# Optimization experiments

Hardware: AMD Instinct MI355X
Metric: run time of the kernel (lower is better)

## Reference

```python
import jax, jax.numpy as jnp
import numpy as np

H, KVH, DH = 16, 4, 64
DIM = 1024
SCALE_BASE = 4096  # context_len
EPS = 1e-6


def rmsnorm(x, g):
    return x * jax.lax.rsqrt(jnp.mean(x * x, axis=-1, keepdims=True) + EPS) * g


def rope_tables(n, dh, dtype):
    inv_freq = 1.0 / (10000.0 ** (jnp.arange(0, dh, 2, dtype=jnp.float32) / dh))
    t = jnp.arange(n, dtype=jnp.float32) * (SCALE_BASE / n)
    freqs = t[:, None] * inv_freq[None, :]          # [n, dh/2]
    emb = jnp.concatenate([freqs, freqs], axis=-1)  # [n, dh]
    return jnp.cos(emb).astype(dtype), jnp.sin(emb).astype(dtype)


def apply_rope(x, cos, sin):
    # x: [b, h, n, dh]; cos/sin: [n, dh]
    x1, x2 = jnp.split(x, 2, axis=-1)
    rot = jnp.concatenate([-x2, x1], axis=-1)
    return x * cos + rot * sin


def setup_inputs() -> dict:
    key = jax.random.key(0)
    ks = jax.random.split(key, 12)
    B, N = 1, 2048
    std = 0.02
    inp = {
        "x": jax.random.normal(ks[0], (B, N, DIM), jnp.float32),
        "a": jax.random.normal(ks[1], (B, N, DIM), jnp.float32),
        "g_x": jnp.ones((DIM,), jnp.float32),
        "g_a": jnp.ones((DIM,), jnp.float32),
        "Wq_x": jax.random.normal(ks[2], (DIM, H * DH), jnp.float32) * std,
        "Wkv_x": jax.random.normal(ks[3], (DIM, 2 * KVH * DH), jnp.float32) * std,
        "Wq_a": jax.random.normal(ks[4], (DIM, H * DH), jnp.float32) * std,
        "Wkv_a": jax.random.normal(ks[5], (DIM, 2 * KVH * DH), jnp.float32) * std,
        "Wout_x": jax.random.normal(ks[6], (H * DH, DIM), jnp.float32) * std,
        "bout_x": jnp.zeros((DIM,), jnp.float32),
        "Wout_a": jax.random.normal(ks[7], (H * DH, DIM), jnp.float32) * std,
        "bout_a": jnp.zeros((DIM,), jnp.float32),
    }
    return inp


def _split_heads(t, h):
    b, n, hd = t.shape
    return t.reshape(b, n, h, hd // h).transpose(0, 2, 1, 3)  # b h n d


def _stream_qkv(s, g, Wq, Wkv):
    s = rmsnorm(s, g)
    q = _split_heads(s @ Wq, H)                 # [b, H, n, DH]
    kv = s @ Wkv
    k, v = jnp.split(kv, 2, axis=-1)
    k = _split_heads(k, KVH)                    # [b, KVH, n, DH]
    v = _split_heads(v, KVH)
    return q, k, v


def reference(x, a, g_x, g_a, Wq_x, Wkv_x, Wq_a, Wkv_a, Wout_x, bout_x, Wout_a, bout_a):
    B, Nx, _ = x.shape
    Na = a.shape[1]
    scale = DH ** -0.5
    r = H // KVH

    q_x, k_x, v_x = _stream_qkv(x, g_x, Wq_x, Wkv_x)
    q_a, k_a, v_a = _stream_qkv(a, g_a, Wq_a, Wkv_a)

    cos_x, sin_x = rope_tables(Nx, DH, x.dtype)
    cos_a, sin_a = rope_tables(Na, DH, a.dtype)
    q_x, k_x = apply_rope(q_x, cos_x, sin_x), apply_rope(k_x, cos_x, sin_x)
    q_a, k_a = apply_rope(q_a, cos_a, sin_a), apply_rope(k_a, cos_a, sin_a)

    # NOTE: original scales q by dim_head**-0.5 AND sdpa scales again -> 1/DH total
    q_x = q_x * scale
    q_a = q_a * scale

    # GQA expansion: einops 'b h n d -> b (r h) n d' == tile heads
    tile = lambda t: jnp.tile(t, (1, r, 1, 1))
    k_x, v_x, k_a, v_a = tile(k_x), tile(v_x), tile(k_a), tile(v_a)

    # pack [a, x] along seq
    q = jnp.concatenate([q_a, q_x], axis=2)
    k = jnp.concatenate([k_a, k_x], axis=2)
    v = jnp.concatenate([v_a, v_x], axis=2)

    scores = jnp.einsum('bhqd,bhkd->bhqk', q, k) * scale  # sdpa's own scale
    attn = jax.nn.softmax(scores, axis=-1)
    out = jnp.einsum('bhqk,bhkd->bhqd', attn, v)          # [b, H, Na+Nx, DH]

    out_a, out_x = out[:, :, :Na], out[:, :, Na:]
    merge = lambda t: t.transpose(0, 2, 1, 3).reshape(B, -1, H * DH)
    out_x = merge(out_x) @ Wout_x + bout_x
    out_a = merge(out_a) @ Wout_a + bout_a
    return out_x, out_a
```

## Files before the change

### kernel.cpp

```cpp
#include <hip/hip_runtime.h>
#include <hip/hip_bf16.h>
#include <stdint.h>
#include <math.h>


#define NSEQ 2048
#define NJ   4096
#define DIMM 1024

typedef __attribute__((ext_vector_type(4))) float f32x4;
typedef __attribute__((ext_vector_type(8))) short bf16x8;
typedef __attribute__((ext_vector_type(4))) short bf16x4;

__device__ __forceinline__ unsigned short f2bf(float f) {
  union { float f; uint32_t u; } v; v.f = f;
  return (unsigned short)((v.u + 0x7FFFu + ((v.u >> 16) & 1u)) >> 16);
}

__device__ __forceinline__ uint32_t pack2bf(float a, float b) {
  __hip_bfloat162 h = __float22bfloat162_rn(float2{a, b});
  union { __hip_bfloat162 h; uint32_t u; } c; c.h = h;
  return c.u;
}

#if defined(__has_builtin)
#if __has_builtin(__builtin_amdgcn_exp2f)
#define FAST_EXP2(x) __builtin_amdgcn_exp2f(x)
#endif
#endif
#ifndef FAST_EXP2
#define FAST_EXP2(x) exp2f(x)
#endif

__device__ __forceinline__ void glds16(const void* g, void* l) {
  __builtin_amdgcn_global_load_lds(
      (const __attribute__((address_space(1))) unsigned int*)g,
      (__attribute__((address_space(3))) unsigned int*)l, 16, 0, 0);
}

__global__ __launch_bounds__(256) void prep_kernel(
    const float* __restrict__ xa, const float* __restrict__ xx,
    const float* __restrict__ ga, const float* __restrict__ gx,
    const float* __restrict__ wqa, const float* __restrict__ wqx,
    const float* __restrict__ wkva, const float* __restrict__ wkvx,
    const float* __restrict__ woa, const float* __restrict__ wox,
    unsigned short* __restrict__ XN, unsigned short* __restrict__ WQT,
    unsigned short* __restrict__ WKVT, unsigned short* __restrict__ WOT,
    float* __restrict__ cosT, float* __restrict__ sinT) {
  __shared__ float tile[32][33];
  __shared__ float red[4];
  int bid = blockIdx.x, t = threadIdx.x;
  if (bid < 256) {
    int idx = bid * 256 + t;
    int pos = idx >> 5, i = idx & 31;
    double inv = pow(10000.0, -(double)i / 32.0);
    double ang = (double)(2 * pos) * inv;
    cosT[idx] = (float)cos(ang);
    sinT[idx] = (float)sin(ang);
  } else if (bid < 6400) {
    int b = bid - 256;
    int z = b >> 10, yx = b & 1023;
    int n0 = (yx >> 5) * 32, k0 = (yx & 31) * 32;
    int s = z & 1, ty = z >> 1;
    int N = (ty == 1) ? 512 : 1024;
    if (n0 >= N) return;
    const float* src = (z == 0) ? wqa : (z == 1) ? wqx : (z == 2) ? wkva
                     : (z == 3) ? wkvx : (z == 4) ? woa : wox;
    unsigned short* dst = (ty == 0) ? WQT + (size_t)s * 1024 * 1024
                        : (ty == 1) ? WKVT + (size_t)s * 512 * 1024
                                    : WOT + (size_t)s * 1024 * 1024;
    int r = t >> 3, c4 = (t & 7) * 4;
    f32x4 v = *(const f32x4*)(src + (size_t)(k0 + r) * N + n0 + c4);
    tile[r][c4 + 0] = v.x; tile[r][c4 + 1] = v.y;
    tile[r][c4 + 2] = v.z; tile[r][c4 + 3] = v.w;
    __syncthreads();
    int nn = t >> 3, kk = (t & 7) * 4;
    bf16x4 o;
    o.x = (short)f2bf(tile[kk + 0][nn]);
    o.y = (short)f2bf(tile[kk + 1][nn]);
    o.z = (short)f2bf(tile[kk + 2][nn]);
    o.w = (short)f2bf(tile[kk + 3][nn]);
    *(bf16x4*)(dst + (size_t)(n0 + nn) * 1024 + k0 + kk) = o;
  } else {
    int b = bid - 6400;
    int s = b >> 11, row = b & 2047;
    const float* src = (s == 0 ? xa : xx) + (size_t)row * DIMM;
    const float* g = (s == 0 ? ga : gx);
    f32x4 v = *(const f32x4*)(src + t * 4);
    float ss = v.x * v.x + v.y * v.y + v.z * v.z + v.w * v.w;
#pragma unroll
    for (int o = 32; o > 0; o >>= 1) ss += __shfl_xor(ss, o, 64);
    if ((t & 63) == 0) red[t >> 6] = ss;
    __syncthreads();
    float tot = red[0] + red[1] + red[2] + red[3];
    float rs = rsqrtf(tot * (1.0f / DIMM) + 1e-6f);
    f32x4 gv = *(const f32x4*)(g + t * 4);
    bf16x4 o;
    o.x = (short)f2bf(v.x * rs * gv.x);
    o.y = (short)f2bf(v.y * rs * gv.y);
    o.z = (short)f2bf(v.z * rs * gv.z);
    o.w = (short)f2bf(v.w * rs * gv.w);
    *(bf16x4*)(XN + ((size_t)s * NSEQ + row) * DIMM + t * 4) = o;
  }
}

__device__ __forceinline__ void gemm64_mainloop(
    const unsigned short* __restrict__ Ag, const unsigned short* __restrict__ Bg,
    unsigned short* As, unsigned short* Bs, f32x4 acc[2][4]) {
  int t = threadIdx.x;
  int lane = t & 63, wid = t >> 6;
  int wm = (wid >> 1) * 32, wn = (wid & 1) * 64;
  int l15 = lane & 15, quad = lane >> 4;
  int srow = t >> 2, sko = (t & 3) * 8;
  const unsigned short* ga = Ag + (size_t)srow * 1024 + sko;
  const unsigned short* gb = Bg + (size_t)srow * 1024 + sko;
  unsigned short* la = As + t * 8;
  unsigned short* lb = Bs + t * 8;
#pragma unroll
  for (int mi = 0; mi < 2; ++mi)
#pragma unroll
    for (int j = 0; j < 4; ++j) acc[mi][j] = (f32x4){0.f, 0.f, 0.f, 0.f};

#define GQ_STAGE(S, KT) do {                                               \
    int k0_ = (KT) * 32;                                                   \
    glds16(ga + k0_, la + (S) * 2048);                                     \
    glds16(gb + k0_, lb + (S) * 4096);                                     \
    glds16(gb + 64 * 1024 + k0_, lb + (S) * 4096 + 2048);                  \
  } while (0)

#define GQ_COMP(S) do {                                                    \
    bf16x8 af[2], bfr[4];                                                  \
    _Pragma("unroll")                                                      \
    for (int mi = 0; mi < 2; ++mi)                                         \
      af[mi] = *(const bf16x8*)(As + (S) * 2048 + (wm + mi * 16 + l15) * 32 + quad * 8); \
    _Pragma("unroll")                                                      \
    for (int j = 0; j < 4; ++j)                                            \
      bfr[j] = *(const bf16x8*)(Bs + (S) * 4096 + (wn + j * 16 + l15) * 32 + quad * 8); \
    _Pragma("unroll")                                                      \
    for (int mi = 0; mi < 2; ++mi)                                         \
      _Pragma("unroll")                                                    \
      for (int j = 0; j < 4; ++j)                                          \
        acc[mi][j] = __builtin_amdgcn_mfma_f32_16x16x32_bf16(af[mi], bfr[j], acc[mi][j], 0, 0, 0); \
  } while (0)

  GQ_STAGE(0, 0);
  GQ_STAGE(1, 1);
  __syncthreads();
  for (int kq = 0; kq < 32; kq += 4) {
    GQ_STAGE(2, (kq + 2) & 31);
    GQ_STAGE(3, (kq + 3) & 31);
    GQ_COMP(0);
    GQ_COMP(1);
    __syncthreads();
    GQ_STAGE(0, (kq + 4) & 31);
    GQ_STAGE(1, (kq + 5) & 31);
    GQ_COMP(2);
    GQ_COMP(3);
    __syncthreads();
  }
#undef GQ_STAGE
#undef GQ_COMP
}

__global__ __launch_bounds__(256) void gemm_qkv_kernel(
    const unsigned short* __restrict__ XN, const unsigned short* __restrict__ WQT,
    const unsigned short* __restrict__ WKVT, const float* __restrict__ cosT,
    const float* __restrict__ sinT, unsigned short* __restrict__ QB,
    unsigned short* __restrict__ KB, unsigned short* __restrict__ VT) {
  __shared__ unsigned short As[4 * 2048], Bs[4 * 4096];
  int n0 = blockIdx.x * 128, m0 = blockIdx.y * 64;
  int s = (m0 >= 2048) ? 1 : 0;
  const unsigned short* Ag = XN + (size_t)m0 * 1024;
  const unsigned short* Bg = (n0 < 1024)
      ? WQT + (size_t)s * 1024 * 1024 + (size_t)n0 * 1024
      : WKVT + (size_t)s * 512 * 1024 + (size_t)(n0 - 1024) * 1024;
  f32x4 acc[2][4];
  gemm64_mainloop(Ag, Bg, As, Bs, acc);
  int t = threadIdx.x, lane = t & 63, wid = t >> 6;
  int wm = (wid >> 1) * 32, wn = (wid & 1) * 64;
  int l15 = lane & 15, quad = lane >> 4;
  int coln = n0 + wn;
  if (coln < 1280) {
    bool isq = coln < 1024;
    float sc = isq ? (1.4426950408889634f / 64.0f) : 1.0f;
    unsigned short* dstBase;
    if (isq) dstBase = QB + (size_t)(coln >> 6) * NJ * 64;
    else     dstBase = KB + (size_t)((coln - 1024) >> 6) * NJ * 64;
#pragma unroll
    for (int mi = 0; mi < 2; ++mi)
#pragma unroll
      for (int r = 0; r < 4; ++r) {
        int jr = m0 + wm + mi * 16 + quad * 4 + r;
        int pos = jr & 2047;
#pragma unroll
        for (int jp = 0; jp < 2; ++jp) {
          int i = jp * 16 + l15;
          float c = cosT[pos * 32 + i], sn = sinT[pos * 32 + i];
          float x1 = acc[mi][jp][r], x2 = acc[mi][jp + 2][r];
          dstBase[(size_t)jr * 64 + jp * 16 + l15]      = f2bf((x1 * c - x2 * sn) * sc);
          dstBase[(size_t)jr * 64 + 32 + jp * 16 + l15] = f2bf((x2 * c + x1 * sn) * sc);
        }
      }
  } else {
    int cvb = coln - 1280;
#pragma unroll
    for (int mi = 0; mi < 2; ++mi)
#pragma unroll
      for (int j = 0; j < 4; ++j) {
        int d = cvb + j * 16 + l15;
        int jr0 = m0 + wm + mi * 16 + quad * 4;
        union { bf16x4 v; uint32_t u[2]; } pv;
        pv.u[0] = pack2bf(acc[mi][j][0], acc[mi][j][1]);
        pv.u[1] = pack2bf(acc[mi][j][2], acc[mi][j][3]);
        *(bf16x4*)(VT + (size_t)d * NJ + jr0) = pv.v;
      }
  }
}

__global__ __launch_bounds__(256, 2) void attn_kernel(
    const unsigned short* __restrict__ QB, const unsigned short* __restrict__ KB,
    const unsigned short* __restrict__ VT, unsigned short* __restrict__ AT) {
  __shared__ __align__(16) unsigned short Ks[4][4096];
  __shared__ __align__(16) unsigned short Vs[4][4096];
  int h = blockIdx.y, qt = blockIdx.x;
  int hk = h & 3;
  int t = threadIdx.x, lane = t & 63, w = t >> 6;
  int l15 = lane & 15, quad = lane >> 4;
  int qsel = w >> 1, ksel = w & 1;
  int q0 = qt * 128 + qsel * 64;
  bf16x8 qf[4][2];
#pragma unroll
  for (int mi = 0; mi < 4; ++mi) {
    const unsigned short* qp = QB + ((size_t)h * NJ + q0 + mi * 16 + l15) * 64;
    qf[mi][0] = *(const bf16x8*)(qp + quad * 8);
    qf[mi][1] = *(const bf16x8*)(qp + 32 + quad * 8);
  }
  f32x4 oT[4][4];
  f32x4 oL[4];
#pragma unroll
  for (int mi = 0; mi < 4; ++mi) {
    oL[mi] = (f32x4){0.f, 0.f, 0.f, 0.f};
#pragma unroll
    for (int db = 0; db < 4; ++db) oT[mi][db] = (f32x4){0.f, 0.f, 0.f, 0.f};
  }
  bf16x8 vone;
  {
    short one = (l15 == 0) ? (short)0x3F80 : (short)0;
    vone = (bf16x8){one, one, one, one, one, one, one, one};
  }
  const unsigned short* Kg = KB + (size_t)hk * NJ * 64;
  const unsigned short* Vg = VT + (size_t)hk * 64 * NJ;
  int r1 = t >> 3, cx = t & 7;
  int e1 = r1 & 7;
  int c1 = cx ^ e1;
  int gk1 = 32 * (r1 >> 5) + 8 * ((r1 >> 2) & 3) + 4 * ((r1 >> 4) & 1) + (r1 & 3);
  int r2 = r1 + 32;
  int gk2 = 32 * (r2 >> 5) + 8 * ((r2 >> 2) & 3) + 4 * ((r2 >> 4) & 1) + (r2 & 3);
  const unsigned short* sK1 = Kg + (size_t)gk1 * 64 + c1 * 8;
  const unsigned short* sK2 = Kg + (size_t)gk2 * 64 + c1 * 8;
  const unsigned short* sV1 = Vg + (size_t)r1 * NJ + c1 * 8;
  const unsigned short* sV2 = Vg + (size_t)r2 * NJ + c1 * 8;
  int e = l15 & 7;
  int co0 = (quad ^ e) * 8;
  int co1 = ((4 + quad) ^ e) * 8;
  int cov = (((ksel << 2) | quad) ^ e) * 8;
  const unsigned short* kf0p = &Ks[0][(2 * ksel * 16 + l15) * 64] + co0;
  const unsigned short* kf0q = &Ks[0][(2 * ksel * 16 + l15) * 64] + co1;
  const unsigned short* kf1p = kf0p + 16 * 64;
  const unsigned short* kf1q = kf0q + 16 * 64;
  const unsigned short* vap0 = &Vs[0][(0 * 16 + l15) * 64] + cov;
  const unsigned short* vap1 = &Vs[0][(1 * 16 + l15) * 64] + cov;
  const unsigned short* vap2 = &Vs[0][(2 * 16 + l15) * 64] + cov;
  const unsigned short* vap3 = &Vs[0][(3 * 16 + l15) * 64] + cov;

  f32x4 sxA[4][2], sxB[4][2];
  bf16x8 pbA[4], pbB[4];

#define STAGE(S, T) do {                                                   \
    size_t ko_ = (size_t)(T) * 4096;                                       \
    int vo_ = (T) * 64;                                                    \
    glds16(sK1 + ko_, &Ks[S][0] + t * 8);                                  \
    glds16(sK2 + ko_, &Ks[S][2048] + t * 8);                               \
    glds16(sV1 + vo_, &Vs[S][0] + t * 8);                                  \
    glds16(sV2 + vo_, &Vs[S][2048] + t * 8);                               \
  } while (0)

#define QK4(S, SX) do {                                                    \
    bf16x8 k00 = *(const bf16x8*)(kf0p + (S) * 4096);                      \
    bf16x8 k01 = *(const bf16x8*)(kf0q + (S) * 4096);                      \
    bf16x8 k10 = *(const bf16x8*)(kf1p + (S) * 4096);                      \
    bf16x8 k11 = *(const bf16x8*)(kf1q + (S) * 4096);                      \
    _Pragma("unroll")                                                      \
    for (int mi = 0; mi < 4; ++mi) {                                       \
      f32x4 z0 = (f32x4){0.f, 0.f, 0.f, 0.f};                              \
      z0 = __builtin_amdgcn_mfma_f32_16x16x32_bf16(k00, qf[mi][0], z0, 0, 0, 0); \
      z0 = __builtin_amdgcn_mfma_f32_16x16x32_bf16(k01, qf[mi][1], z0, 0, 0, 0); \
      (SX)[mi][0] = z0;                                                    \
      f32x4 z1 = (f32x4){0.f, 0.f, 0.f, 0.f};                              \
      z1 = __builtin_amdgcn_mfma_f32_16x16x32_bf16(k10, qf[mi][0], z1, 0, 0, 0); \
      z1 = __builtin_amdgcn_mfma_f32_16x16x32_bf16(k11, qf[mi][1], z1, 0, 0, 0); \
      (SX)[mi][1] = z1;                                                    \
    }                                                                      \
  } while (0)

#define PHASE_A(SQ, SXN, SXP, PB) do {                                     \
    bf16x8 k00 = *(const bf16x8*)(kf0p + (SQ) * 4096);                     \
    bf16x8 k01 = *(const bf16x8*)(kf0q + (SQ) * 4096);                     \
    bf16x8 k10 = *(const bf16x8*)(kf1p + (SQ) * 4096);                     \
    bf16x8 k11 = *(const bf16x8*)(kf1q + (SQ) * 4096);                     \
    _Pragma("unroll")                                                      \
    for (int mi = 0; mi < 4; ++mi) {                                       \
      f32x4 z0 = (f32x4){0.f, 0.f, 0.f, 0.f};                              \
      z0 = __builtin_amdgcn_mfma_f32_16x16x32_bf16(k00, qf[mi][0], z0, 0, 0, 0); \
      z0 = __builtin_amdgcn_mfma_f32_16x16x32_bf16(k01, qf[mi][1], z0, 0, 0, 0); \
      (SXN)[mi][0] = z0;                                                   \
      f32x4 z1 = (f32x4){0.f, 0.f, 0.f, 0.f};                              \
      z1 = __builtin_amdgcn_mfma_f32_16x16x32_bf16(k10, qf[mi][0], z1, 0, 0, 0); \
      z1 = __builtin_amdgcn_mfma_f32_16x16x32_bf16(k11, qf[mi][1], z1, 0, 0, 0); \
      (SXN)[mi][1] = z1;                                                   \
      union { bf16x8 v; uint32_t u[4]; } pk_;                              \
      pk_.u[0] = pack2bf(FAST_EXP2((SXP)[mi][0][0]), FAST_EXP2((SXP)[mi][0][1])); \
      pk_.u[1] = pack2bf(FAST_EXP2((SXP)[mi][0][2]), FAST_EXP2((SXP)[mi][0][3])); \
      pk_.u[2] = pack2bf(FAST_EXP2((SXP)[mi][1][0]), FAST_EXP2((SXP)[mi][1][1])); \
      pk_.u[3] = pack2bf(FAST_EXP2((SXP)[mi][1][2]), FAST_EXP2((SXP)[mi][1][3])); \
      (PB)[mi] = pk_.v;                                                    \
    }                                                                      \
  } while (0)

#define PHASE_C(SP, PB, SX, PBN) do {                                      \
    bf16x8 va0 = *(const bf16x8*)(vap0 + (SP) * 4096);                     \
    bf16x8 va1 = *(const bf16x8*)(vap1 + (SP) * 4096);                     \
    bf16x8 va2 = *(const bf16x8*)(vap2 + (SP) * 4096);                     \
    bf16x8 va3 = *(const bf16x8*)(vap3 + (SP) * 4096);                     \
    _Pragma("unroll")                                                      \
    for (int mi = 0; mi < 4; ++mi) {                                       \
      oT[mi][0] = __builtin_amdgcn_mfma_f32_16x16x32_bf16(va0, (PB)[mi], oT[mi][0], 0, 0, 0); \
      oT[mi][1] = __builtin_amdgcn_mfma_f32_16x16x32_bf16(va1, (PB)[mi], oT[mi][1], 0, 0, 0); \
      oT[mi][2] = __builtin_amdgcn_mfma_f32_16x16x32_bf16(va2, (PB)[mi], oT[mi][2], 0, 0, 0); \
      oT[mi][3] = __builtin_amdgcn_mfma_f32_16x16x32_bf16(va3, (PB)[mi], oT[mi][3], 0, 0, 0); \
      oL[mi]    = __builtin_amdgcn_mfma_f32_16x16x32_bf16(vone, (PB)[mi], oL[mi], 0, 0, 0); \
      union { bf16x8 v; uint32_t u[4]; } pk_;                              \
      pk_.u[0] = pack2bf(FAST_EXP2((SX)[mi][0][0]), FAST_EXP2((SX)[mi][0][1])); \
      pk_.u[1] = pack2bf(FAST_EXP2((SX)[mi][0][2]), FAST_EXP2((SX)[mi][0][3])); \
      pk_.u[2] = pack2bf(FAST_EXP2((SX)[mi][1][0]), FAST_EXP2((SX)[mi][1][1])); \
      pk_.u[3] = pack2bf(FAST_EXP2((SX)[mi][1][2]), FAST_EXP2((SX)[mi][1][3])); \
      (PBN)[mi] = pk_.v;                                                   \
    }                                                                      \
  } while (0)

#define PHASE_B(SP, PB) do {                                               \
    __builtin_amdgcn_s_setprio(1);                                         \
    {                                                                      \
      bf16x8 va0 = *(const bf16x8*)(vap0 + (SP) * 4096);                   \
      bf16x8 va1 = *(const bf16x8*)(vap1 + (SP) * 4096);                   \
      bf16x8 va2 = *(const bf16x8*)(vap2 + (SP) * 4096);                   \
      bf16x8 va3 = *(const bf16x8*)(vap3 + (SP) * 4096);                   \
      _Pragma("unroll")                                                    \
      for (int mi = 0; mi < 4; ++mi) {                                     \
        oT[mi][0] = __builtin_amdgcn_mfma_f32_16x16x32_bf16(va0, (PB)[mi], oT[mi][0], 0, 0, 0); \
        oT[mi][1] = __builtin_amdgcn_mfma_f32_16x16x32_bf16(va1, (PB)[mi], oT[mi][1], 0, 0, 0); \
        oT[mi][2] = __builtin_amdgcn_mfma_f32_16x16x32_bf16(va2, (PB)[mi], oT[mi][2], 0, 0, 0); \
        oT[mi][3] = __builtin_amdgcn_mfma_f32_16x16x32_bf16(va3, (PB)[mi], oT[mi][3], 0, 0, 0); \
        oL[mi]    = __builtin_amdgcn_mfma_f32_16x16x32_bf16(vone, (PB)[mi], oL[mi], 0, 0, 0); \
      }                                                                    \
    }                                                                      \
    __builtin_amdgcn_s_setprio(0);                                         \
  } while (0)

  STAGE(0, 0);
  STAGE(1, 1);
  __syncthreads();
  for (int P = 0; P < 16; ++P) {
    int tb = 4 * P;
    STAGE(2, (tb + 2) & 63);
    STAGE(3, (tb + 3) & 63);
    QK4(0, sxA);
    PHASE_A(1, sxB, sxA, pbA);
    PHASE_C(0, pbA, sxB, pbB);
    PHASE_B(1, pbB);
    __syncthreads();
    STAGE(0, (tb + 4) & 63);
    STAGE(1, (tb + 5) & 63);
    QK4(2, sxA);
    PHASE_A(3, sxB, sxA, pbA);
    PHASE_C(2, pbA, sxB, pbB);
    PHASE_B(3, pbB);
    __syncthreads();
  }
#undef STAGE
#undef QK4
#undef PHASE_A
#undef PHASE_C
#undef PHASE_B

  float ls[4];
#pragma unroll
  for (int mi = 0; mi < 4; ++mi) {
    float s = oL[mi][0];
    s += __shfl_xor(s, 16, 64);
    s += __shfl_xor(s, 32, 64);
    ls[mi] = s;
  }
  float* xb = (qsel == 0) ? (float*)&Ks[0][0] : (float*)&Vs[0][0];
  float* xl = xb + 64 * 68;
  if (ksel == 1) {
    f32x4* dst = (f32x4*)xb + (size_t)lane * 17;
#pragma unroll
    for (int mi = 0; mi < 4; ++mi)
#pragma unroll
      for (int db = 0; db < 4; ++db) dst[mi * 4 + db] = oT[mi][db];
    float* dl = xl + lane * 4;
#pragma unroll
    for (int mi = 0; mi < 4; ++mi) dl[mi] = ls[mi];
  }
  __syncthreads();
  if (ksel == 0) {
    const f32x4* src = (const f32x4*)xb + (size_t)lane * 17;
    const float* sl = xl + lane * 4;
#pragma unroll
    for (int mi = 0; mi < 4; ++mi) {
      float inv = 1.0f / (ls[mi] + sl[mi]);
      int qrow = q0 + mi * 16 + l15;
#pragma unroll
      for (int db = 0; db < 4; ++db) {
        f32x4 o = oT[mi][db] + src[mi * 4 + db];
        union { bf16x4 v; uint32_t u[2]; } ov;
        ov.u[0] = pack2bf(o[0] * inv, o[1] * inv);
        ov.u[1] = pack2bf(o[2] * inv, o[3] * inv);
        *(bf16x4*)(AT + (size_t)qrow * DIMM + h * 64 + db * 16 + quad * 4) = ov.v;
      }
    }
  }
}

__global__ __launch_bounds__(256) void gemm_out_kernel(
    const unsigned short* __restrict__ AT, const unsigned short* __restrict__ WOT,
    const float* __restrict__ ba, const float* __restrict__ bx,
    float* __restrict__ out) {
  __shared__ unsigned short As[4 * 2048], Bs[4 * 4096];
  int n0 = blockIdx.x * 128, m0 = blockIdx.y * 64;
  int s = (m0 >= 2048) ? 1 : 0;
  const unsigned short* Ag = AT + (size_t)m0 * 1024;
  const unsigned short* Bg = WOT + (size_t)s * 1024 * 1024 + (size_t)n0 * 1024;
  f32x4 acc[2][4];
  gemm64_mainloop(Ag, Bg, As, Bs, acc);
  int t = threadIdx.x, lane = t & 63, wid = t >> 6;
  int wm = (wid >> 1) * 32, wn = (wid & 1) * 64;
  int l15 = lane & 15, quad = lane >> 4;
  const float* bias = s ? bx : ba;
  float* obase = s ? (out + (size_t)(m0 - 2048) * 1024)
                   : (out + (size_t)2048 * 1024 + (size_t)m0 * 1024);
#pragma unroll
  for (int mi = 0; mi < 2; ++mi)
#pragma unroll
    for (int r = 0; r < 4; ++r) {
      int row = wm + mi * 16 + quad * 4 + r;
#pragma unroll
      for (int j = 0; j < 4; ++j) {
        int col = n0 + wn + j * 16 + l15;
        obase[(size_t)row * 1024 + col] = acc[mi][j][r] + bias[col];
      }
    }
}

extern "C" void kernel_launch(void* const* d_in, const int* in_sizes, int n_in,
                              void* d_out, int out_size, void* d_ws, size_t ws_size,
                              hipStream_t stream) {
  const float* x      = (const float*)d_in[0];
  const float* a      = (const float*)d_in[1];
  const float* g_x    = (const float*)d_in[2];
  const float* g_a    = (const float*)d_in[3];
  const float* Wq_x   = (const float*)d_in[4];
  const float* Wkv_x  = (const float*)d_in[5];
  const float* Wq_a   = (const float*)d_in[6];
  const float* Wkv_a  = (const float*)d_in[7];
  const float* Wout_x = (const float*)d_in[8];
  const float* bout_x = (const float*)d_in[9];
  const float* Wout_a = (const float*)d_in[10];
  const float* bout_a = (const float*)d_in[11];
  float* out = (float*)d_out;

  char* ws = (char*)d_ws;
  const size_t MB = 1024 * 1024;
  unsigned short* XN   = (unsigned short*)(ws);
  unsigned short* WQT  = (unsigned short*)(ws + 8 * MB);
  unsigned short* WKVT = (unsigned short*)(ws + 12 * MB);
  unsigned short* WOT  = (unsigned short*)(ws + 14 * MB);
  unsigned short* QB   = (unsigned short*)(ws + 18 * MB);
  unsigned short* KB   = (unsigned short*)(ws + 26 * MB);
  unsigned short* VT   = (unsigned short*)(ws + 28 * MB);
  float* cosT          = (float*)(ws + 30 * MB);
  float* sinT          = (float*)(ws + 30 * MB + 262144);
  unsigned short* AT   = XN;

  prep_kernel<<<dim3(10496), dim3(256), 0, stream>>>(
      a, x, g_a, g_x, Wq_a, Wq_x, Wkv_a, Wkv_x, Wout_a, Wout_x,
      XN, WQT, WKVT, WOT, cosT, sinT);
  gemm_qkv_kernel<<<dim3(12, 64), dim3(256), 0, stream>>>(
      XN, WQT, WKVT, cosT, sinT, QB, KB, VT);
  attn_kernel<<<dim3(32, 16), dim3(256), 0, stream>>>(QB, KB, VT, AT);
  gemm_out_kernel<<<dim3(8, 64), dim3(256), 0, stream>>>(
      AT, WOT, bout_a, bout_x, out);
}
```

Baseline: 218.3 us.

## Restructure attention loop into continuous software pipeline and use hardware sin/cos for RoPE

The attention main loop is rebuilt as a steady-state software pipeline. QK for the next tile is computed alongside the exp and PV of the previous tile, with one barrier per tile instead of a burst of two stages per barrier, and a single P buffer replaces the two. This aims to overlap MFMA work with the softmax exponentials and spread LDS staging more evenly, but doubles the number of barriers. Separately, the RoPE table prep swaps double-precision pow/sin/cos for a bitwise product of constants and the hardware v_sin/v_cos instructions, cutting prep cost at some loss of precision.

```diff
diff --git a/kernel.cpp b/kernel.cpp
--- a/kernel.cpp
+++ b/kernel.cpp
@@ -53,10 +53,21 @@
   if (bid < 256) {
     int idx = bid * 256 + t;
     int pos = idx >> 5, i = idx & 31;
-    double inv = pow(10000.0, -(double)i / 32.0);
+    double inv = 1.0;
+    if (i & 1)  inv *= 0.74989420933245582;
+    if (i & 2)  inv *= 0.56234132519034908;
+    if (i & 4)  inv *= 0.31622776601683794;
+    if (i & 8)  inv *= 0.1;
+    if (i & 16) inv *= 0.01;
     double ang = (double)(2 * pos) * inv;
-    cosT[idx] = (float)cos(ang);
-    sinT[idx] = (float)sin(ang);
+    double rev = ang * 0.15915494309189535;
+    rev -= floor(rev);
+    float rf = (float)rev;
+    float c, s;
+    asm("v_cos_f32 %0, %1" : "=v"(c) : "v"(rf));
+    asm("v_sin_f32 %0, %1" : "=v"(s) : "v"(rf));
+    cosT[idx] = c;
+    sinT[idx] = s;
   } else if (bid < 6400) {
     int b = bid - 256;
     int z = b >> 10, yx = b & 1023;
@@ -274,7 +285,7 @@
   const unsigned short* vap3 = &Vs[0][(3 * 16 + l15) * 64] + cov;
 
   f32x4 sxA[4][2], sxB[4][2];
-  bf16x8 pbA[4], pbB[4];
+  bf16x8 pb[4];
 
 #define STAGE(S, T) do {                                                   \
     size_t ko_ = (size_t)(T) * 4096;                                       \
@@ -303,7 +314,7 @@
     }                                                                      \
   } while (0)
 
-#define PHASE_A(SQ, SXN, SXP, PB) do {                                     \
+#define PHASE_A(SQ, SXN, SXP) do {                                         \
     bf16x8 k00 = *(const bf16x8*)(kf0p + (SQ) * 4096);                     \
     bf16x8 k01 = *(const bf16x8*)(kf0q + (SQ) * 4096);                     \
     bf16x8 k10 = *(const bf16x8*)(kf1p + (SQ) * 4096);                     \
@@ -323,32 +334,11 @@
       pk_.u[1] = pack2bf(FAST_EXP2((SXP)[mi][0][2]), FAST_EXP2((SXP)[mi][0][3])); \
       pk_.u[2] = pack2bf(FAST_EXP2((SXP)[mi][1][0]), FAST_EXP2((SXP)[mi][1][1])); \
       pk_.u[3] = pack2bf(FAST_EXP2((SXP)[mi][1][2]), FAST_EXP2((SXP)[mi][1][3])); \
-      (PB)[mi] = pk_.v;                                                    \
+      pb[mi] = pk_.v;                                                      \
     }                                                                      \
   } while (0)
 
-#define PHASE_C(SP, PB, SX, PBN) do {                                      \
-    bf16x8 va0 = *(const bf16x8*)(vap0 + (SP) * 4096);                     \
-    bf16x8 va1 = *(const bf16x8*)(vap1 + (SP) * 4096);                     \
-    bf16x8 va2 = *(const bf16x8*)(vap2 + (SP) * 4096);                     \
-    bf16x8 va3 = *(const bf16x8*)(vap3 + (SP) * 4096);                     \
-    _Pragma("unroll")                                                      \
-    for (int mi = 0; mi < 4; ++mi) {                                       \
-      oT[mi][0] = __builtin_amdgcn_mfma_f32_16x16x32_bf16(va0, (PB)[mi], oT[mi][0], 0, 0, 0); \
-      oT[mi][1] = __builtin_amdgcn_mfma_f32_16x16x32_bf16(va1, (PB)[mi], oT[mi][1], 0, 0, 0); \
-      oT[mi][2] = __builtin_amdgcn_mfma_f32_16x16x32_bf16(va2, (PB)[mi], oT[mi][2], 0, 0, 0); \
-      oT[mi][3] = __builtin_amdgcn_mfma_f32_16x16x32_bf16(va3, (PB)[mi], oT[mi][3], 0, 0, 0); \
-      oL[mi]    = __builtin_amdgcn_mfma_f32_16x16x32_bf16(vone, (PB)[mi], oL[mi], 0, 0, 0); \
-      union { bf16x8 v; uint32_t u[4]; } pk_;                              \
-      pk_.u[0] = pack2bf(FAST_EXP2((SX)[mi][0][0]), FAST_EXP2((SX)[mi][0][1])); \
-      pk_.u[1] = pack2bf(FAST_EXP2((SX)[mi][0][2]), FAST_EXP2((SX)[mi][0][3])); \
-      pk_.u[2] = pack2bf(FAST_EXP2((SX)[mi][1][0]), FAST_EXP2((SX)[mi][1][1])); \
-      pk_.u[3] = pack2bf(FAST_EXP2((SX)[mi][1][2]), FAST_EXP2((SX)[mi][1][3])); \
-      (PBN)[mi] = pk_.v;                                                   \
-    }                                                                      \
-  } while (0)
-
-#define PHASE_B(SP, PB) do {                                               \
+#define PHASE_B(SP) do {                                                   \
     __builtin_amdgcn_s_setprio(1);                                         \
     {                                                                      \
       bf16x8 va0 = *(const bf16x8*)(vap0 + (SP) * 4096);                   \
@@ -357,11 +347,11 @@
       bf16x8 va3 = *(const bf16x8*)(vap3 + (SP) * 4096);                   \
       _Pragma("unroll")                                                    \
       for (int mi = 0; mi < 4; ++mi) {                                     \
-        oT[mi][0] = __builtin_amdgcn_mfma_f32_16x16x32_bf16(va0, (PB)[mi], oT[mi][0], 0, 0, 0); \
-        oT[mi][1] = __builtin_amdgcn_mfma_f32_16x16x32_bf16(va1, (PB)[mi], oT[mi][1], 0, 0, 0); \
-        oT[mi][2] = __builtin_amdgcn_mfma_f32_16x16x32_bf16(va2, (PB)[mi], oT[mi][2], 0, 0, 0); \
-        oT[mi][3] = __builtin_amdgcn_mfma_f32_16x16x32_bf16(va3, (PB)[mi], oT[mi][3], 0, 0, 0); \
-        oL[mi]    = __builtin_amdgcn_mfma_f32_16x16x32_bf16(vone, (PB)[mi], oL[mi], 0, 0, 0); \
+        oT[mi][0] = __builtin_amdgcn_mfma_f32_16x16x32_bf16(va0, pb[mi], oT[mi][0], 0, 0, 0); \
+        oT[mi][1] = __builtin_amdgcn_mfma_f32_16x16x32_bf16(va1, pb[mi], oT[mi][1], 0, 0, 0); \
+        oT[mi][2] = __builtin_amdgcn_mfma_f32_16x16x32_bf16(va2, pb[mi], oT[mi][2], 0, 0, 0); \
+        oT[mi][3] = __builtin_amdgcn_mfma_f32_16x16x32_bf16(va3, pb[mi], oT[mi][3], 0, 0, 0); \
+        oL[mi] = __builtin_amdgcn_mfma_f32_16x16x32_bf16(vone, pb[mi], oL[mi], 0, 0, 0); \
       }                                                                    \
     }                                                                      \
     __builtin_amdgcn_s_setprio(0);                                         \
@@ -370,27 +360,29 @@
   STAGE(0, 0);
   STAGE(1, 1);
   __syncthreads();
+  QK4(0, sxA);
   for (int P = 0; P < 16; ++P) {
     int tb = 4 * P;
     STAGE(2, (tb + 2) & 63);
+    PHASE_A(1, sxB, sxA);
+    PHASE_B(0);
+    __syncthreads();
     STAGE(3, (tb + 3) & 63);
-    QK4(0, sxA);
-    PHASE_A(1, sxB, sxA, pbA);
-    PHASE_C(0, pbA, sxB, pbB);
-    PHASE_B(1, pbB);
+    PHASE_A(2, sxA, sxB);
+    PHASE_B(1);
     __syncthreads();
     STAGE(0, (tb + 4) & 63);
+    PHASE_A(3, sxB, sxA);
+    PHASE_B(2);
+    __syncthreads();
     STAGE(1, (tb + 5) & 63);
-    QK4(2, sxA);
-    PHASE_A(3, sxB, sxA, pbA);
-    PHASE_C(2, pbA, sxB, pbB);
-    PHASE_B(3, pbB);
+    PHASE_A(0, sxA, sxB);
+    PHASE_B(3);
     __syncthreads();
   }
 #undef STAGE
 #undef QK4
 #undef PHASE_A
-#undef PHASE_C
 #undef PHASE_B
 
   float ls[4];
```

Result: no change. 219.5 us (+0.6%).
